# Kernel tuning notes

Hardware: AMD Instinct MI355X
Metric: run time of the kernel (lower is better)

## Reference

```python
import jax, jax.numpy as jnp
import numpy as np

H, E, V, F, P, B = 512, 512, 10000, 1280, 196, 32
SOS = 1

def setup_inputs() -> dict:
    key = jax.random.key(0)
    ks = jax.random.split(key, 24)
    s = 0.02
    return {
        "feature_outputs": jax.random.normal(ks[0], (B, P, F), jnp.float32),
        "caption": jax.random.randint(ks[1], (B, 80), 0, V),
        "max_caption": 80,
        "embedding": jax.random.normal(ks[2], (V, E), jnp.float32) * s,
        "W1_w": jax.random.normal(ks[3], (H, H), jnp.float32) * s,
        "W1_b": jnp.full((H,), 0.01, jnp.float32),
        "W2_w": jax.random.normal(ks[4], (H, F), jnp.float32) * s,
        "W2_b": jnp.full((H,), 0.01, jnp.float32),
        "Va_w": jax.random.normal(ks[5], (1, H), jnp.float32) * s,
        "Va_b": jnp.full((1,), 0.01, jnp.float32),
        "lstm_Wih": jax.random.normal(ks[6], (4 * H, E + F), jnp.float32) * s,
        "lstm_Whh": jax.random.normal(ks[7], (4 * H, H), jnp.float32) * s,
        "lstm_bih": jnp.zeros((4 * H,), jnp.float32),
        "lstm_bhh": jnp.zeros((4 * H,), jnp.float32),
        "out_w": jax.random.normal(ks[8], (V, H), jnp.float32) * s,
        "out_b": jnp.full((V,), 0.01, jnp.float32),
        "init_h_w": jax.random.normal(ks[9], (H, F), jnp.float32) * s,
        "init_h_b": jnp.full((H,), 0.01, jnp.float32),
        "init_c_w": jax.random.normal(ks[10], (H, F), jnp.float32) * s,
        "init_c_b": jnp.full((H,), 0.01, jnp.float32),
        "gate_w": jax.random.normal(ks[11], (F, H), jnp.float32) * s,
        "gate_b": jnp.full((F,), 0.01, jnp.float32),
    }


def reference(feature_outputs, caption, max_caption, embedding,
              W1_w, W1_b, W2_w, W2_b, Va_w, Va_b,
              lstm_Wih, lstm_Whh, lstm_bih, lstm_bhh,
              out_w, out_b, init_h_w, init_h_b, init_c_w, init_c_b,
              gate_w, gate_b):
    steps = int(max_caption)
    bsz = caption.shape[0]
    mean_enc = feature_outputs.mean(axis=1)                       # [B,F]
    h0 = mean_enc @ init_h_w.T + init_h_b                         # [B,H]
    c0 = mean_enc @ init_c_w.T + init_c_b                         # [B,H]
    # W2(keys) is constant across steps -> hoist out of the loop
    enc_proj = jnp.einsum('bpf,hf->bph', feature_outputs, W2_w) + W2_b  # [B,P,H]
    inp0 = jnp.broadcast_to(embedding[SOS], (bsz, embedding.shape[1]))  # [B,E]

    def step(carry, _):
        h, c, inp = carry
        # Bahdanau attention
        hid = h @ W1_w.T + W1_b                                   # [B,H]
        scores = (jax.nn.relu(hid[:, None, :] + enc_proj) @ Va_w[0] + Va_b[0])  # [B,P]
        weights = jax.nn.softmax(scores, axis=1)
        context = jnp.einsum('bpf,bp->bf', feature_outputs, weights)  # [B,F]
        gate = jax.nn.sigmoid(h @ gate_w.T + gate_b)              # [B,F]
        context = context * gate
        # LSTMCell (torch gate order: i, f, g, o)
        x = jnp.concatenate([inp, context], axis=1)               # [B,E+F]
        gates = x @ lstm_Wih.T + lstm_bih + h @ lstm_Whh.T + lstm_bhh
        i_g, f_g, g_g, o_g = jnp.split(gates, 4, axis=1)
        c_new = jax.nn.sigmoid(f_g) * c + jax.nn.sigmoid(i_g) * jnp.tanh(g_g)
        h_new = jax.nn.sigmoid(o_g) * jnp.tanh(c_new)
        logits = h_new @ out_w.T + out_b                          # [B,V] (dropout = eval identity)
        nxt = embedding[jnp.argmax(logits, axis=-1)]              # greedy decode
        return (h_new, c_new, nxt), (logits, weights)

    (h, c, _), (outs, attns) = jax.lax.scan(step, (h0, c0, inp0), None, length=steps)
    decoder_outputs = jnp.transpose(outs, (1, 0, 2))              # [B,T,V]
    attentions = jnp.transpose(attns, (1, 0, 2))                  # [B,T,P]
    return decoder_outputs, (h, c), attentions
```

## Files before the change

kernel.cpp:

```cpp
#include <hip/hip_runtime.h>
#include <hip/hip_cooperative_groups.h>
#include <math.h>

#define RI __restrict__

namespace {

constexpr int Hn=512, En=512, Vn=10000, Fn=1280, Pn=196, Bn=32, Tn=80;
constexpr int G4 = 2048, KX = 1792;
constexpr int NCAT = 13888;
constexpr int NVT = 157;
constexpr int J_GATE = 512, J_XP = 1792, J_LOG = 3840;
constexpr int NBLK = 256;
constexpr int XROW = 140;

constexpr long O_ENC  = 0;
constexpr long O_W2T  = O_ENC  + (long)Bn*Pn*Hn;
constexpr long O_WCAT = O_W2T  + (long)Fn*Hn;
constexpr long O_WIHT = O_WCAT + (long)Hn*NCAT;
constexpr long O_C    = O_WIHT + (long)KX*G4;
constexpr long O_HT   = O_C    + (long)Bn*Hn;
constexpr long O_HID  = O_HT   + (long)Hn*Bn;
constexpr long O_GT   = O_HID  + (long)Bn*Hn;
constexpr long O_XPT  = O_GT   + (long)Bn*Fn;
constexpr long O_XT   = O_XPT  + (long)G4*Bn;
constexpr long O_PMV  = O_XT   + (long)Bn*KX;
constexpr long O_PMI  = O_PMV  + (long)Bn*NVT;
constexpr long O_SVAL = O_PMI  + (long)Bn*NVT;
constexpr long O_SEL  = O_SVAL + (long)Bn*Pn;
constexpr long O_CNT  = O_SEL  + 64;
constexpr long O_IHCT  = O_ENC;
constexpr long O_MEANT = O_ENC + (long)Fn*1024;

__device__ __forceinline__ float sigm(float x){ return 1.0f/(1.0f+expf(-x)); }
__device__ __forceinline__ void fma4(float4& a, const float4 x, const float w){
  a.x += w*x.x; a.y += w*x.y; a.z += w*x.z; a.w += w*x.w;
}
__device__ __forceinline__ float ldc(const float* p){
  return __hip_atomic_load(p, __ATOMIC_RELAXED, __HIP_MEMORY_SCOPE_AGENT);
}
__device__ __forceinline__ void stc(float* p, float v){
  __hip_atomic_store(p, v, __ATOMIC_RELAXED, __HIP_MEMORY_SCOPE_AGENT);
}
__device__ __forceinline__ int ldci(const int* p){
  return __hip_atomic_load(p, __ATOMIC_RELAXED, __HIP_MEMORY_SCOPE_AGENT);
}
__device__ __forceinline__ void stci(int* p, int v){
  __hip_atomic_store(p, v, __ATOMIC_RELAXED, __HIP_MEMORY_SCOPE_AGENT);
}
__device__ __forceinline__ float2 ldc2(const float* p){
  union { unsigned long long u; float2 f; } c;
  c.u = __hip_atomic_load((const unsigned long long*)p,
                          __ATOMIC_RELAXED, __HIP_MEMORY_SCOPE_AGENT);
  return c.f;
}
__device__ __forceinline__ unsigned ldcu(const unsigned* p){
  return __hip_atomic_load(p, __ATOMIC_RELAXED, __HIP_MEMORY_SCOPE_AGENT);
}
__device__ __forceinline__ void incc(unsigned* p){
  __hip_atomic_fetch_add(p, 1u, __ATOMIC_RELAXED, __HIP_MEMORY_SCOPE_AGENT);
}

__device__ __forceinline__ void w1(const unsigned* a, unsigned ta){
  if (threadIdx.x == 0){
    while (ldcu(a) < ta) __builtin_amdgcn_s_sleep(2);
  }
  __syncthreads();
}
__device__ __forceinline__ void w3(const unsigned* a, unsigned ta,
                                   const unsigned* b, unsigned tb,
                                   const unsigned* c, unsigned tc){
  if (threadIdx.x == 0){
    while (ldcu(a) < ta || ldcu(b) < tb || ldcu(c) < tc) __builtin_amdgcn_s_sleep(2);
  }
  __syncthreads();
}

__global__ __launch_bounds__(256) void k_tr_s(const float* RI src, float* RI dst,
                                              int R, int C, int S){
  __shared__ float t[32][33];
  int tc0 = blockIdx.x*32, tr0 = blockIdx.y*32;
  int lx = threadIdx.x & 31, ly = threadIdx.x >> 5;
  for (int i = ly; i < 32; i += 8){
    int r = tr0 + i, c = tc0 + lx;
    t[i][lx] = (r < R && c < C) ? src[(long)r*C + c] : 0.f;
  }
  __syncthreads();
  for (int i = ly; i < 32; i += 8){
    int c = tc0 + i, r = tr0 + lx;
    if (c < C && r < R) dst[(long)c*S + r] = t[lx][i];
  }
}

__global__ __launch_bounds__(256) void k_tr_wih(const float* RI src, float* RI ws){
  __shared__ float t[32][33];
  int tk0 = blockIdx.x*32, tj0 = blockIdx.y*32;
  int lx = threadIdx.x & 31, ly = threadIdx.x >> 5;
  for (int i = ly; i < 32; i += 8){
    int j = tj0 + i, k = tk0 + lx;
    t[i][lx] = src[(long)j*KX + k];
  }
  __syncthreads();
  for (int i = ly; i < 32; i += 8){
    int k = tk0 + i, j = tj0 + lx;
    int pc = ((j & 511) << 2) | (j >> 9);
    ws[O_WIHT + ((long)(pc >> 3)*KX + k)*8 + (pc & 7)] = t[lx][i];
  }
}

__global__ __launch_bounds__(256) void k_mean(const float* RI feat, float* RI ws){
  int blk = blockIdx.x;
  int b = blk / 5, ft = blk % 5;
  int f = ft*256 + threadIdx.x;
  float s = 0.f;
  const float* fp = feat + (long)b*Pn*Fn + f;
  for (int p = 0; p < Pn; ++p) s += fp[(long)p*Fn];
  ws[O_MEANT + (long)f*Bn + b] = s * (1.0f/Pn);
}

__global__ __launch_bounds__(512) void k_h0c0(const float* RI ihb, const float* RI icb,
                                              float* RI ws){
  int tid = threadIdx.x;
  int jl = tid & 63, bq = tid >> 6;
  int j = blockIdx.x*64 + jl;
  const float* wp = ws + O_IHCT + j;
  const float* xp = ws + O_MEANT + bq*4;
  float4 acc = make_float4(0,0,0,0);
  for (int k = 0; k < Fn; ++k){
    float w = wp[(long)k*1024];
    float4 x = *(const float4*)(xp + (long)k*Bn);
    fma4(acc, x, w);
  }
  float va[4] = {acc.x, acc.y, acc.z, acc.w};
  if (j < Hn){
    float bias = ihb[j];
    #pragma unroll
    for (int m = 0; m < 4; ++m)
      ws[O_HT + (long)j*Bn + (bq*4+m)] = va[m] + bias;
  } else {
    int j2 = j - Hn;
    float bias = icb[j2];
    #pragma unroll
    for (int m = 0; m < 4; ++m)
      ws[O_C + (long)(bq*4+m)*Hn + j2] = va[m] + bias;
  }
}

__global__ __launch_bounds__(512) void k_encproj(const float* RI feat, const float* RI w2b,
                                                 float* RI ws){
  __shared__ __align__(16) float xs[64*65];
  const int blk = blockIdx.x;
  const int rt = blk >> 2, ct = blk & 3;
  const int r0 = rt*64, j0 = ct*128;
  const int tid = threadIdx.x;
  const int jq = tid & 31, rg = tid >> 5;
  const int rw = tid >> 3, kc = (tid & 7)*8;
  const float* w2t = ws + O_W2T + j0 + jq*4;
  float4 a0 = make_float4(0,0,0,0), a1 = a0, a2 = a0, a3 = a0;
  for (int k0 = 0; k0 < Fn; k0 += 64){
    __syncthreads();
    {
      const float* fp = feat + (long)(r0+rw)*Fn + k0 + kc;
      float4 v0 = *(const float4*)(fp);
      float4 v1 = *(const float4*)(fp + 4);
      float* xr = xs + rw*65 + kc;
      xr[0]=v0.x; xr[1]=v0.y; xr[2]=v0.z; xr[3]=v0.w;
      xr[4]=v1.x; xr[5]=v1.y; xr[6]=v1.z; xr[7]=v1.w;
    }
    __syncthreads();
    #pragma unroll 4
    for (int kk = 0; kk < 64; ++kk){
      float4 w = *(const float4*)(w2t + (long)(k0+kk)*Hn);
      const float* xp = xs + (rg*4)*65 + kk;
      fma4(a0, w, xp[0]);
      fma4(a1, w, xp[65]);
      fma4(a2, w, xp[130]);
      fma4(a3, w, xp[195]);
    }
  }
  float4 b4 = *(const float4*)(w2b + j0 + jq*4);
  float4 out[4] = {a0,a1,a2,a3};
  #pragma unroll
  for (int m = 0; m < 4; ++m){
    long r = r0 + rg*4 + m;
    float4 o = out[m];
    o.x += b4.x; o.y += b4.y; o.z += b4.z; o.w += b4.w;
    *(float4*)(ws + O_ENC + r*Hn + j0 + jq*4) = o;
  }
}

__global__ __launch_bounds__(512) void k_decode(
    const float* RI feat, const float* RI emb, const float* RI vaw, const float* RI vab,
    const float* RI w1b, const float* RI gb, const float* RI bih, const float* RI bhh,
    const float* RI outb, float* RI ws, float* RI dout)
{
  __shared__ __align__(16) float wlds[32768];
  __shared__ __align__(16) float sbuf[4608];
  const int blk = blockIdx.x, tid = threadIdx.x;
  const int jl = tid & 63, bq = tid >> 6;
  unsigned* cnt = (unsigned*)(ws + O_CNT);
  unsigned* C_H   = cnt + 0;
  unsigned* C_P1  = cnt + 32;
  unsigned* C_HID = cnt + 64;
  unsigned* C_GT  = cnt + 96;
  unsigned* C_XP  = cnt + 128;
  unsigned* C_LOG = cnt + 160;
  unsigned* C_XT  = cnt + 192;
  #define C_SC(b)  (cnt + 256 + (b)*8)
  #define C_SEL(b) (cnt + 512 + (b)*8)

  if (blk < 217){
    const float* wg = ws + O_WCAT + blk*64;
    for (int idx = tid; idx < 512*64; idx += 512){
      int k = idx >> 6, j = idx & 63;
      wlds[idx] = wg[(long)k*NCAT + j];
    }
  }
  __syncthreads();

  for (int t = 0; t <= Tn; ++t){
    if (blk < 217){
      if (t > 0) w1(C_H, 256u*t);
      bool p1act = (t == Tn) ? (blk >= 60) : !(t == 0 && blk >= 60);
      if (p1act){
        float4 acc = make_float4(0,0,0,0);
        float2 pre0 = ldc2(ws + O_HT + tid*2);
        float2 pre1 = ldc2(ws + O_HT + 1024 + tid*2);
        for (int c8 = 0; c8 < 8; ++c8){
          __syncthreads();
          *(float2*)(sbuf + tid*2) = pre0;
          *(float2*)(sbuf + 1024 + tid*2) = pre1;
          __syncthreads();
          if (c8 < 7){
            pre0 = ldc2(ws + O_HT + (long)(c8+1)*2048 + tid*2);
            pre1 = ldc2(ws + O_HT + (long)(c8+1)*2048 + 1024 + tid*2);
          }
          #pragma unroll 8
          for (int kk = 0; kk < 64; ++kk){
            float w = wlds[(long)(c8*64 + kk)*64 + jl];
            float4 x = *(const float4*)(sbuf + kk*32 + bq*4);
            fma4(acc, x, w);
          }
        }
        __syncthreads();
        const int j = blk*64 + jl;
        if (blk < 8){
          float bias = w1b[j];
          stc(ws + O_HID + (long)(bq*4+0)*Hn + j, acc.x + bias);
          stc(ws + O_HID + (long)(bq*4+1)*Hn + j, acc.y + bias);
          stc(ws + O_HID + (long)(bq*4+2)*Hn + j, acc.z + bias);
          stc(ws + O_HID + (long)(bq*4+3)*Hn + j, acc.w + bias);
        } else if (blk < 28){
          int f = j - J_GATE;
          float bias = gb[f];
          stc(ws + O_GT + (long)(bq*4+0)*Fn + f, sigm(acc.x + bias));
          stc(ws + O_GT + (long)(bq*4+1)*Fn + f, sigm(acc.y + bias));
          stc(ws + O_GT + (long)(bq*4+2)*Fn + f, sigm(acc.z + bias));
          stc(ws + O_GT + (long)(bq*4+3)*Fn + f, sigm(acc.w + bias));
        } else if (blk < 60){
          int j2 = j - J_XP;
          float bias = bih[j2] + bhh[j2];
          sbuf[jl*33 + bq*4+0] = acc.x + bias;
          sbuf[jl*33 + bq*4+1] = acc.y + bias;
          sbuf[jl*33 + bq*4+2] = acc.z + bias;
          sbuf[jl*33 + bq*4+3] = acc.w + bias;
          __syncthreads();
          #pragma unroll
          for (int r = 0; r < 4; ++r){
            int idx = r*512 + tid;
            int row = idx >> 5, b = idx & 31;
            int j2r = (blk-28)*64 + row;
            int pc = ((j2r & 511) << 2) | (j2r >> 9);
            stc(ws + O_XPT + (long)pc*Bn + b, sbuf[row*33 + b]);
          }
        } else {
          int v = j - J_LOG;
          float lv[4];
          if (v < Vn){
            float bias = outb[v];
            lv[0]=acc.x+bias; lv[1]=acc.y+bias; lv[2]=acc.z+bias; lv[3]=acc.w+bias;
            #pragma unroll
            for (int m = 0; m < 4; ++m)
              dout[((long)(bq*4+m)*Tn + (t-1))*Vn + v] = lv[m];
          } else {
            lv[0]=lv[1]=lv[2]=lv[3]=-1e30f;
          }
          int tile = blk - 60;
          #pragma unroll
          for (int m = 0; m < 4; ++m){
            float bv = lv[m]; int bi = v;
            #pragma unroll
            for (int off = 32; off; off >>= 1){
              float ov = __shfl_down(bv, off, 64);
              int   oi = __shfl_down(bi, off, 64);
              if (ov > bv || (ov == bv && oi < bi)){ bv = ov; bi = oi; }
            }
            if (jl == 0){
              int b = bq*4 + m;
              stc (ws + O_PMV + (long)b*NVT + tile, bv);
              stci((int*)(ws + O_PMI) + (long)b*NVT + tile, bi);
            }
          }
        }
      }
      __syncthreads();
      if (tid == 0){
        unsigned* role = (blk < 8) ? C_HID : (blk < 28) ? C_GT
                       : (blk < 60) ? C_XP : C_LOG;
        incc(role); incc(C_P1);
      }
    }
    if (t == Tn) break;

    if (blk < 224){
      const int b = blk & 31, part = blk >> 5;
      w1(C_HID, 8u*(t+1));
      float* hid_s = sbuf;
      float* va_s  = sbuf + 512;
      float* sv    = sbuf + 1024;
      hid_s[tid] = ldc(ws + O_HID + (long)b*Hn + tid);
      va_s[tid]  = vaw[tid];
      __syncthreads();
      const int w = tid >> 6, l = tid & 63;
      const int p0 = part*28;
      const float* eb = ws + O_ENC + (long)b*Pn*Hn;
      #pragma unroll 2
      for (int p = p0 + w; p < p0 + 28; p += 8){
        const float* er = eb + (long)p*Hn;
        float4 e0 = *(const float4*)(er + l*4);
        float4 e1 = *(const float4*)(er + 256 + l*4);
        float4 h0 = *(const float4*)(hid_s + l*4);
        float4 h1 = *(const float4*)(hid_s + 256 + l*4);
        float4 v0 = *(const float4*)(va_s + l*4);
        float4 v1 = *(const float4*)(va_s + 256 + l*4);
        float s = fmaxf(h0.x+e0.x,0.f)*v0.x + fmaxf(h0.y+e0.y,0.f)*v0.y
                + fmaxf(h0.z+e0.z,0.f)*v0.z + fmaxf(h0.w+e0.w,0.f)*v0.w
                + fmaxf(h1.x+e1.x,0.f)*v1.x + fmaxf(h1.y+e1.y,0.f)*v1.y
                + fmaxf(h1.z+e1.z,0.f)*v1.z + fmaxf(h1.w+e1.w,0.f)*v1.w;
        #pragma unroll
        for (int off = 32; off; off >>= 1) s += __shfl_down(s, off, 64);
        if (l == 0) sv[p - p0] = s + vab[0];
      }
      __syncthreads();
      if (tid < 28) stc(ws + O_SVAL + (long)b*Pn + p0 + tid, sv[tid]);
      __syncthreads();
      if (tid == 0) incc(C_SC(b));
    } else {
      const int b = blk - 224;
      w1(C_LOG, 157u*(t+1));
      if (t == 0){
        if (tid == 0) stci((int*)(ws + O_SEL) + b, 1);
      } else if (tid < 64){
        float bv = -1e30f; int bi = 0x7fffffff;
        for (int q = tid; q < NVT; q += 64){
          float cv = ldc(ws + O_PMV + (long)b*NVT + q);
          if (cv > bv){ bv = cv; bi = ldci((const int*)(ws + O_PMI) + (long)b*NVT + q); }
        }
        #pragma unroll
        for (int off = 32; off; off >>= 1){
          float ov = __shfl_down(bv, off, 64);
          int   oi = __shfl_down(bi, off, 64);
          if (ov > bv || (ov == bv && oi < bi)){ bv = ov; bi = oi; }
        }
        if (tid == 0) stci((int*)(ws + O_SEL) + b, bi);
      }
      __syncthreads();
      if (tid == 0) incc(C_SEL(b));
    }

    {
      const int b = blk & 31, fr = blk >> 5;
      const int f0 = fr*160;
      w3(C_SC(b), 7u*(t+1), C_SEL(b), (unsigned)(t+1), C_GT, 20u*(t+1));
      float* svl = sbuf;
      float* wts = sbuf + 208;
      if (tid < Pn) svl[tid] = ldc(ws + O_SVAL + (long)b*Pn + tid);
      if (tid == 0) ((int*)sbuf)[450] = ldci((const int*)(ws + O_SEL) + b);
      __syncthreads();
      if (tid < 64){
        float m = -1e30f;
        for (int p = tid; p < Pn; p += 64) m = fmaxf(m, svl[p]);
        #pragma unroll
        for (int off = 32; off; off >>= 1) m = fmaxf(m, __shfl_xor(m, off, 64));
        float sm = 0.f;
        for (int p = tid; p < Pn; p += 64) sm += expf(svl[p] - m);
        #pragma unroll
        for (int off = 32; off; off >>= 1) sm += __shfl_xor(sm, off, 64);
        if (tid == 0){ sbuf[448] = m; sbuf[449] = 1.0f/sm; }
      }
      __syncthreads();
      if (tid < Pn){
        float wv = expf(svl[tid] - sbuf[448]) * sbuf[449];
        wts[tid] = wv;
        if (fr == 0)
          dout[(long)Bn*Tn*Vn + 2L*Bn*Hn + ((long)b*Tn + t)*Pn + tid] = wv;
      }
      __syncthreads();
      const int pp = tid / 160, fl = tid - pp*160;
      float a = 0.f;
      if (tid < 480){
        const int p0 = pp*66, pn = (pp == 2) ? 64 : 66;
        const float* fp = feat + ((long)b*Pn + p0)*Fn + f0 + fl;
        const float* wl = wts + p0;
        float s0=0,s1=0,s2=0,s3=0,s4=0,s5=0,s6=0,s7=0;
        int p = 0;
        for (; p + 8 <= pn; p += 8){
          s0 += wl[p+0]*fp[(long)(p+0)*Fn];
          s1 += wl[p+1]*fp[(long)(p+1)*Fn];
          s2 += wl[p+2]*fp[(long)(p+2)*Fn];
          s3 += wl[p+3]*fp[(long)(p+3)*Fn];
          s4 += wl[p+4]*fp[(long)(p+4)*Fn];
          s5 += wl[p+5]*fp[(long)(p+5)*Fn];
          s6 += wl[p+6]*fp[(long)(p+6)*Fn];
          s7 += wl[p+7]*fp[(long)(p+7)*Fn];
        }
        for (; p < pn; ++p) s0 += wl[p]*fp[(long)p*Fn];
        a = ((s0+s1)+(s2+s3)) + ((s4+s5)+(s6+s7));
        if (pp > 0) sbuf[512 + (pp-1)*160 + fl] = a;
      }
      __syncthreads();
      if (tid < 160){
        float tot = a + sbuf[512 + tid] + sbuf[672 + tid];
        int f = f0 + tid;
        tot *= ldc(ws + O_GT + (long)b*Fn + f);
        stc(ws + O_XT + (long)b*KX + En + f, tot);
      }
      if (fr == 0){
        int row = ((int*)sbuf)[450];
        stc(ws + O_XT + (long)b*KX + tid, emb[(long)row*En + tid]);
      }
      __syncthreads();
      if (tid == 0) incc(C_XT);
    }

    {
      w3(C_XT, 256u*(t+1), C_XP, 32u*(t+1), C_P1, 217u*(t+1));
      const int c = tid & 7, ks = tid >> 3;
      const int pc0 = blk*8;
      const float* wg = ws + O_WIHT + (long)blk*KX*8;
      float4 acc4[8];
      #pragma unroll
      for (int q = 0; q < 8; ++q) acc4[q] = make_float4(0,0,0,0);
      float2 pre[4];
      #pragma unroll
      for (int r = 0; r < 4; ++r){
        int flat = r*1024 + tid*2;
        pre[r] = ldc2(ws + O_XT + (long)(flat >> 7)*KX + (flat & 127));
      }
      for (int ch = 0; ch < 14; ++ch){
        __syncthreads();
        #pragma unroll
        for (int r = 0; r < 4; ++r){
          int flat = r*1024 + tid*2;
          int kl = flat & 127, b = flat >> 7;
          int sc = kl + ((kl >> 5) << 2);
          float* xd = sbuf + b*XROW;
          xd[sc] = pre[r].x; xd[sc+1] = pre[r].y;
        }
        __syncthreads();
        if (ch < 13){
          long k0n = (long)(ch+1)*128;
          #pragma unroll
          for (int r = 0; r < 4; ++r){
            int flat = r*1024 + tid*2;
            pre[r] = ldc2(ws + O_XT + (long)(flat >> 7)*KX + k0n + (flat & 127));
          }
        }
        const long kg0 = (long)ch*128;
        #pragma unroll
        for (int kk = 0; kk < 2; ++kk){
          int kl = ks*2 + kk;
          float w = wg[(kg0 + kl)*8 + c];
          int cs = kl + ((kl >> 5) << 2);
          const float* xq = sbuf + cs;
          #pragma unroll
          for (int q = 0; q < 8; ++q){
            const float* xb = xq + (q*4)*XROW;
            acc4[q].x += w * xb[0];
            acc4[q].y += w * xb[XROW];
            acc4[q].z += w * xb[2*XROW];
            acc4[q].w += w * xb[3*XROW];
          }
        }
      }
      #pragma unroll
      for (int off = 8; off <= 32; off <<= 1){
        #pragma unroll
        for (int q = 0; q < 8; ++q){
          acc4[q].x += __shfl_xor(acc4[q].x, off, 64);
          acc4[q].y += __shfl_xor(acc4[q].y, off, 64);
          acc4[q].z += __shfl_xor(acc4[q].z, off, 64);
          acc4[q].w += __shfl_xor(acc4[q].w, off, 64);
        }
      }
      __syncthreads();
      const int wv = tid >> 6, lane = tid & 63;
      if (lane < 8){
        float* rb = sbuf + (wv*8 + lane)*32;
        #pragma unroll
        for (int q = 0; q < 8; ++q) *(float4*)(rb + q*4) = acc4[q];
      }
      __syncthreads();
      if (tid < 256){
        int cc = tid >> 5, b = tid & 31;
        float s = 0.f;
        #pragma unroll
        for (int w2 = 0; w2 < 8; ++w2) s += sbuf[(w2*8 + cc)*32 + b];
        s += ldc(ws + O_XPT + (long)(pc0 + cc)*Bn + b);
        sbuf[2048 + cc*32 + b] = s;
      }
      __syncthreads();
      if (tid < 64){
        int il = tid >> 5, b = tid & 31;
        int i = blk*2 + il;
        float gi  = sbuf[2048 + (il*4+0)*32 + b];
        float gf  = sbuf[2048 + (il*4+1)*32 + b];
        float gg2 = sbuf[2048 + (il*4+2)*32 + b];
        float go  = sbuf[2048 + (il*4+3)*32 + b];
        float c_ = ws[O_C + (long)b*Hn + i];
        float cn = sigm(gf)*c_ + sigm(gi)*tanhf(gg2);
        float hn = sigm(go)*tanhf(cn);
        ws[O_C + (long)b*Hn + i] = cn;
        stc(ws + O_HT + (long)i*Bn + b, hn);
        if (t == Tn-1){
          dout[(long)Bn*Tn*Vn + (long)b*Hn + i] = hn;
          dout[(long)Bn*Tn*Vn + (long)Bn*Hn + (long)b*Hn + i] = cn;
        }
      }
      __syncthreads();
      if (tid == 0) incc(C_H);
    }
  }
  #undef C_SC
  #undef C_SEL
}

}

extern "C" void kernel_launch(void* const* d_in, const int* in_sizes, int n_in,
                              void* d_out, int out_size, void* d_ws, size_t ws_size,
                              hipStream_t stream)
{
  (void)in_sizes; (void)n_in; (void)out_size; (void)ws_size;
  const float* feat = (const float*)d_in[0];
  const float* emb  = (const float*)d_in[3];
  const float* w1w  = (const float*)d_in[4];
  const float* w1b  = (const float*)d_in[5];
  const float* w2w  = (const float*)d_in[6];
  const float* w2b  = (const float*)d_in[7];
  const float* vaw  = (const float*)d_in[8];
  const float* vab  = (const float*)d_in[9];
  const float* wih  = (const float*)d_in[10];
  const float* whh  = (const float*)d_in[11];
  const float* bih  = (const float*)d_in[12];
  const float* bhh  = (const float*)d_in[13];
  const float* outw = (const float*)d_in[14];
  const float* outb = (const float*)d_in[15];
  const float* ihw  = (const float*)d_in[16];
  const float* ihb  = (const float*)d_in[17];
  const float* icw  = (const float*)d_in[18];
  const float* icb  = (const float*)d_in[19];
  const float* gw   = (const float*)d_in[20];
  const float* gb   = (const float*)d_in[21];
  float* ws  = (float*)d_ws;
  float* out = (float*)d_out;

  hipMemsetAsync((char*)d_ws + O_CNT*sizeof(float), 0, 4096, stream);

  k_tr_s<<<dim3(40,16),  256, 0, stream>>>(ihw,  ws + O_IHCT,       Hn, Fn, 1024);
  k_tr_s<<<dim3(40,16),  256, 0, stream>>>(icw,  ws + O_IHCT + 512, Hn, Fn, 1024);
  k_mean<<<160, 256, 0, stream>>>(feat, ws);
  k_h0c0<<<16, 512, 0, stream>>>(ihb, icb, ws);
  k_tr_s<<<dim3(16,16),  256, 0, stream>>>(w1w,  ws + O_WCAT,          Hn, Hn, NCAT);
  k_tr_s<<<dim3(16,40),  256, 0, stream>>>(gw,   ws + O_WCAT + J_GATE, Fn, Hn, NCAT);
  k_tr_s<<<dim3(16,64),  256, 0, stream>>>(whh,  ws + O_WCAT + J_XP,   G4, Hn, NCAT);
  k_tr_s<<<dim3(16,313), 256, 0, stream>>>(outw, ws + O_WCAT + J_LOG,  Vn, Hn, NCAT);
  k_tr_wih<<<dim3(56,64), 256, 0, stream>>>(wih, ws);
  k_tr_s<<<dim3(40,16),  256, 0, stream>>>(w2w,  ws + O_W2T,           Hn, Fn, Hn);
  k_encproj<<<392, 512, 0, stream>>>(feat, w2b, ws);

  void* kargs[] = { (void*)&feat, (void*)&emb, (void*)&vaw, (void*)&vab,
                    (void*)&w1b, (void*)&gb, (void*)&bih, (void*)&bhh,
                    (void*)&outb, (void*)&ws, (void*)&out };
  hipLaunchCooperativeKernel((const void*)k_decode, dim3(NBLK), dim3(512),
                             kargs, 0, stream);
}
```

Measured before the change: 5.624 ms.

## Register-tile phase-1 GEMV with split-K lanes and padded LDS layouts

Reworks the per-step hidden-state matmul in the persistent decode kernel. Each thread now computes a 4x4 (output x batch) register tile over a quarter of K, reading float4 weights and activations from LDS with padded strides to avoid bank conflicts. Partial sums are combined with cross-lane shuffles. Results are staged through LDS so the epilogue can do vectorized 64-bit and float4 global stores and a 16-lane argmax. The aim is more FMAs per LDS load; the cost is higher register pressure and extra shuffle and LDS synchronization work.

```diff
diff --git a/kernel.cpp b/kernel.cpp
--- a/kernel.cpp
+++ b/kernel.cpp
@@ -13,6 +13,7 @@
 constexpr int J_GATE = 512, J_XP = 1792, J_LOG = 3840;
 constexpr int NBLK = 256;
 constexpr int XROW = 140;
+constexpr int WPAD = 66;
 
 constexpr long O_ENC  = 0;
 constexpr long O_W2T  = O_ENC  + (long)Bn*Pn*Hn;
@@ -41,6 +42,12 @@
 }
 __device__ __forceinline__ void stc(float* p, float v){
   __hip_atomic_store(p, v, __ATOMIC_RELAXED, __HIP_MEMORY_SCOPE_AGENT);
+}
+__device__ __forceinline__ void stc2(float* p, float a, float b){
+  union { float f[2]; unsigned long long u; } c;
+  c.f[0] = a; c.f[1] = b;
+  __hip_atomic_store((unsigned long long*)p, c.u,
+                     __ATOMIC_RELAXED, __HIP_MEMORY_SCOPE_AGENT);
 }
 __device__ __forceinline__ int ldci(const int* p){
   return __hip_atomic_load(p, __ATOMIC_RELAXED, __HIP_MEMORY_SCOPE_AGENT);
@@ -194,10 +201,9 @@
     const float* RI w1b, const float* RI gb, const float* RI bih, const float* RI bhh,
     const float* RI outb, float* RI ws, float* RI dout)
 {
-  __shared__ __align__(16) float wlds[32768];
+  __shared__ __align__(16) float wlds[512*WPAD];
   __shared__ __align__(16) float sbuf[4608];
   const int blk = blockIdx.x, tid = threadIdx.x;
-  const int jl = tid & 63, bq = tid >> 6;
   unsigned* cnt = (unsigned*)(ws + O_CNT);
   unsigned* C_H   = cnt + 0;
   unsigned* C_P1  = cnt + 32;
@@ -213,7 +219,7 @@
     const float* wg = ws + O_WCAT + blk*64;
     for (int idx = tid; idx < 512*64; idx += 512){
       int k = idx >> 6, j = idx & 63;
-      wlds[idx] = wg[(long)k*NCAT + j];
+      wlds[k*WPAD + j] = wg[(long)k*NCAT + j];
     }
   }
   __syncthreads();
@@ -223,83 +229,113 @@
       if (t > 0) w1(C_H, 256u*t);
       bool p1act = (t == Tn) ? (blk >= 60) : !(t == 0 && blk >= 60);
       if (p1act){
-        float4 acc = make_float4(0,0,0,0);
+        const int lane = tid & 63, wv0 = tid >> 6;
+        const int ks = lane >> 4, sub = lane & 15;
+        const int jq = (wv0 >> 1)*4 + (sub >> 2);
+        const int bq = (wv0 & 1)*4 + (sub & 3);
+        float4 acc0 = make_float4(0,0,0,0), acc1 = acc0, acc2 = acc0, acc3 = acc0;
         float2 pre0 = ldc2(ws + O_HT + tid*2);
         float2 pre1 = ldc2(ws + O_HT + 1024 + tid*2);
+        const int k0a = (tid*2) >> 5, ba = (tid*2) & 31;
+        const int k1a = k0a + 32;
         for (int c8 = 0; c8 < 8; ++c8){
           __syncthreads();
-          *(float2*)(sbuf + tid*2) = pre0;
-          *(float2*)(sbuf + 1024 + tid*2) = pre1;
+          sbuf[k0a*40 + ba]     = pre0.x;
+          sbuf[k0a*40 + ba + 1] = pre0.y;
+          sbuf[k1a*40 + ba]     = pre1.x;
+          sbuf[k1a*40 + ba + 1] = pre1.y;
           __syncthreads();
           if (c8 < 7){
             pre0 = ldc2(ws + O_HT + (long)(c8+1)*2048 + tid*2);
             pre1 = ldc2(ws + O_HT + (long)(c8+1)*2048 + 1024 + tid*2);
           }
-          #pragma unroll 8
-          for (int kk = 0; kk < 64; ++kk){
-            float w = wlds[(long)(c8*64 + kk)*64 + jl];
-            float4 x = *(const float4*)(sbuf + kk*32 + bq*4);
-            fma4(acc, x, w);
-          }
-        }
+          const float* wb = wlds + (long)(c8*64 + ks)*WPAD + jq*4;
+          const float* xb = sbuf + ks*40 + bq*4;
+          #pragma unroll
+          for (int i = 0; i < 16; ++i){
+            float4 w4 = *(const float4*)(wb + i*(4*WPAD));
+            float4 x4 = *(const float4*)(xb + i*160);
+            fma4(acc0, x4, w4.x); fma4(acc1, x4, w4.y);
+            fma4(acc2, x4, w4.z); fma4(acc3, x4, w4.w);
+          }
+        }
+        #pragma unroll
+        for (int off = 16; off <= 32; off <<= 1){
+          acc0.x += __shfl_xor(acc0.x, off, 64); acc0.y += __shfl_xor(acc0.y, off, 64);
+          acc0.z += __shfl_xor(acc0.z, off, 64); acc0.w += __shfl_xor(acc0.w, off, 64);
+          acc1.x += __shfl_xor(acc1.x, off, 64); acc1.y += __shfl_xor(acc1.y, off, 64);
+          acc1.z += __shfl_xor(acc1.z, off, 64); acc1.w += __shfl_xor(acc1.w, off, 64);
+          acc2.x += __shfl_xor(acc2.x, off, 64); acc2.y += __shfl_xor(acc2.y, off, 64);
+          acc2.z += __shfl_xor(acc2.z, off, 64); acc2.w += __shfl_xor(acc2.w, off, 64);
+          acc3.x += __shfl_xor(acc3.x, off, 64); acc3.y += __shfl_xor(acc3.y, off, 64);
+          acc3.z += __shfl_xor(acc3.z, off, 64); acc3.w += __shfl_xor(acc3.w, off, 64);
+        }
+        float4 av = acc0;
+        if (ks == 1) av = acc1;
+        else if (ks == 2) av = acc2;
+        else if (ks == 3) av = acc3;
         __syncthreads();
-        const int j = blk*64 + jl;
+        {
+          int j = jq*4 + ks;
+          float* row = sbuf + j*33 + bq*4;
+          row[0] = av.x; row[1] = av.y; row[2] = av.z; row[3] = av.w;
+        }
+        __syncthreads();
+        const int eb = tid >> 4, eh = tid & 15;
         if (blk < 8){
-          float bias = w1b[j];
-          stc(ws + O_HID + (long)(bq*4+0)*Hn + j, acc.x + bias);
-          stc(ws + O_HID + (long)(bq*4+1)*Hn + j, acc.y + bias);
-          stc(ws + O_HID + (long)(bq*4+2)*Hn + j, acc.z + bias);
-          stc(ws + O_HID + (long)(bq*4+3)*Hn + j, acc.w + bias);
+          int j4 = eh*4, jg = blk*64 + j4;
+          float h0 = sbuf[(j4+0)*33 + eb] + w1b[jg+0];
+          float h1 = sbuf[(j4+1)*33 + eb] + w1b[jg+1];
+          float h2 = sbuf[(j4+2)*33 + eb] + w1b[jg+2];
+          float h3 = sbuf[(j4+3)*33 + eb] + w1b[jg+3];
+          stc2(ws + O_HID + (long)eb*Hn + jg,     h0, h1);
+          stc2(ws + O_HID + (long)eb*Hn + jg + 2, h2, h3);
         } else if (blk < 28){
-          int f = j - J_GATE;
-          float bias = gb[f];
-          stc(ws + O_GT + (long)(bq*4+0)*Fn + f, sigm(acc.x + bias));
-          stc(ws + O_GT + (long)(bq*4+1)*Fn + f, sigm(acc.y + bias));
-          stc(ws + O_GT + (long)(bq*4+2)*Fn + f, sigm(acc.z + bias));
-          stc(ws + O_GT + (long)(bq*4+3)*Fn + f, sigm(acc.w + bias));
+          int j4 = eh*4, f0 = (blk-8)*64 + j4;
+          float g0 = sigm(sbuf[(j4+0)*33 + eb] + gb[f0+0]);
+          float g1 = sigm(sbuf[(j4+1)*33 + eb] + gb[f0+1]);
+          float g2 = sigm(sbuf[(j4+2)*33 + eb] + gb[f0+2]);
+          float g3 = sigm(sbuf[(j4+3)*33 + eb] + gb[f0+3]);
+          stc2(ws + O_GT + (long)eb*Fn + f0,     g0, g1);
+          stc2(ws + O_GT + (long)eb*Fn + f0 + 2, g2, g3);
         } else if (blk < 60){
-          int j2 = j - J_XP;
-          float bias = bih[j2] + bhh[j2];
-          sbuf[jl*33 + bq*4+0] = acc.x + bias;
-          sbuf[jl*33 + bq*4+1] = acc.y + bias;
-          sbuf[jl*33 + bq*4+2] = acc.z + bias;
-          sbuf[jl*33 + bq*4+3] = acc.w + bias;
-          __syncthreads();
           #pragma unroll
           for (int r = 0; r < 4; ++r){
             int idx = r*512 + tid;
             int row = idx >> 5, b = idx & 31;
             int j2r = (blk-28)*64 + row;
             int pc = ((j2r & 511) << 2) | (j2r >> 9);
-            stc(ws + O_XPT + (long)pc*Bn + b, sbuf[row*33 + b]);
+            stc(ws + O_XPT + (long)pc*Bn + b,
+                sbuf[row*33 + b] + bih[j2r] + bhh[j2r]);
           }
         } else {
-          int v = j - J_LOG;
-          float lv[4];
-          if (v < Vn){
-            float bias = outb[v];
-            lv[0]=acc.x+bias; lv[1]=acc.y+bias; lv[2]=acc.z+bias; lv[3]=acc.w+bias;
-            #pragma unroll
-            for (int m = 0; m < 4; ++m)
-              dout[((long)(bq*4+m)*Tn + (t-1))*Vn + v] = lv[m];
+          int tile = blk - 60;
+          int v0 = tile*64 + eh*4;
+          float lv0, lv1, lv2, lv3;
+          if (v0 < Vn){
+            int j4 = eh*4;
+            lv0 = sbuf[(j4+0)*33 + eb] + outb[v0+0];
+            lv1 = sbuf[(j4+1)*33 + eb] + outb[v0+1];
+            lv2 = sbuf[(j4+2)*33 + eb] + outb[v0+2];
+            lv3 = sbuf[(j4+3)*33 + eb] + outb[v0+3];
+            float4 o = make_float4(lv0, lv1, lv2, lv3);
+            *(float4*)(dout + ((long)eb*Tn + (t-1))*Vn + v0) = o;
           } else {
-            lv[0]=lv[1]=lv[2]=lv[3]=-1e30f;
-          }
-          int tile = blk - 60;
+            lv0 = lv1 = lv2 = lv3 = -1e30f;
+          }
+          float bv = lv0; int bi = v0;
+          if (lv1 > bv){ bv = lv1; bi = v0+1; }
+          if (lv2 > bv){ bv = lv2; bi = v0+2; }
+          if (lv3 > bv){ bv = lv3; bi = v0+3; }
           #pragma unroll
-          for (int m = 0; m < 4; ++m){
-            float bv = lv[m]; int bi = v;
-            #pragma unroll
-            for (int off = 32; off; off >>= 1){
-              float ov = __shfl_down(bv, off, 64);
-              int   oi = __shfl_down(bi, off, 64);
-              if (ov > bv || (ov == bv && oi < bi)){ bv = ov; bi = oi; }
-            }
-            if (jl == 0){
-              int b = bq*4 + m;
-              stc (ws + O_PMV + (long)b*NVT + tile, bv);
-              stci((int*)(ws + O_PMI) + (long)b*NVT + tile, bi);
-            }
+          for (int off = 8; off; off >>= 1){
+            float ov = __shfl_down(bv, off, 16);
+            int   oi = __shfl_down(bi, off, 16);
+            if (ov > bv || (ov == bv && oi < bi)){ bv = ov; bi = oi; }
+          }
+          if (eh == 0){
+            stc (ws + O_PMV + (long)eb*NVT + tile, bv);
+            stci((int*)(ws + O_PMI) + (long)eb*NVT + tile, bi);
           }
         }
       }
```

Result: slower. 6.848 ms (+21.8%).
